# Performance work log

Measured on AMD Instinct MI355X. Metric: run time of the kernel, lower is better.

Reference implementation:

```python
import jax, jax.numpy as jnp
import numpy as np

B, N, E = 2, 2048, 1024   # batch, seq_len, embed_dim (= hidden_dim)
H, HD = 16, 64            # num_heads, head_dim


def setup_inputs() -> dict:
    key = jax.random.key(0)
    ks = jax.random.split(key, 6)
    w = lambda k: jax.random.normal(k, (E, E), jnp.float32) * 0.02
    return {
        "x": jax.random.normal(ks[0], (B, N, E), jnp.float32),
        "Wq": w(ks[1]), "bq": jnp.zeros((E,), jnp.float32),
        "Wk": w(ks[2]), "bk": jnp.zeros((E,), jnp.float32),
        "Wv": w(ks[3]), "bv": jnp.zeros((E,), jnp.float32),
        "Wu": w(ks[4]), "bu": jnp.zeros((E,), jnp.float32),
        "Wo": w(ks[5]), "bo": jnp.zeros((E,), jnp.float32),
        "ln_g": jnp.ones((E,), jnp.float32),
        "ln_b": jnp.zeros((E,), jnp.float32),
    }


def reference(x, Wq, bq, Wk, bk, Wv, bv, Wu, bu, Wo, bo, ln_g, ln_b):
    # projections (torch Linear: x @ W.T + b)
    q = x @ Wq.T + bq
    k = x @ Wk.T + bk
    v = jax.nn.silu(x @ Wv.T + bv)   # uv_act = swish
    u = jax.nn.silu(x @ Wu.T + bu)
    # split heads: [B, N, H*HD] -> [B, H, N, HD]
    split = lambda t: t.reshape(B, N, H, HD).transpose(0, 2, 1, 3)
    q, k, v = split(q), split(k), split(v)
    # non-softmax attention: ReLU on scaled energy (no causal mask)
    energy = jnp.einsum("bhnd,bhmd->bhnm", q, k) / jnp.float32(np.sqrt(HD))
    energy = jax.nn.relu(energy)
    out = jnp.einsum("bhnm,bhmd->bhnd", energy, v)
    # merge heads: [B, H, N, HD] -> [B, N, H*HD]
    out = out.transpose(0, 2, 1, 3).reshape(B, N, H * HD)
    # layernorm over hidden_dim
    mu = out.mean(-1, keepdims=True)
    var = out.var(-1, keepdims=True)
    out = (out - mu) * jax.lax.rsqrt(var + 1e-5) * ln_g + ln_b
    # gate and output projection
    out = u * out
    return out @ Wo.T + bo
```

## Files before the change

kernel.cpp:

```cpp
#include <hip/hip_runtime.h>
#include <stdint.h>

typedef unsigned short u16;
typedef __attribute__((ext_vector_type(8))) short short8;
typedef __attribute__((ext_vector_type(4))) short short4v;
typedef __attribute__((ext_vector_type(4))) float floatx4;
typedef __attribute__((ext_vector_type(4))) int intx4;

#define B_ 2
#define N_ 2048
#define E_ 1024
#define H_ 16
#define HD_ 64
#define M_TOT (B_ * N_)

__device__ __forceinline__ float bf2f(u16 h) {
    union { unsigned u; float f; } c; c.u = ((unsigned)h) << 16; return c.f;
}
__device__ __forceinline__ u16 f2bf(float f) {
    union { float f; unsigned u; } c; c.f = f;
    unsigned r = c.u + 0x7FFFu + ((c.u >> 16) & 1u);
    return (u16)(r >> 16);
}
__device__ __forceinline__ float silu_f(float x) { return x / (1.f + __expf(-x)); }

template <typename T> __device__ __forceinline__ void store_out(T* p, float v);
template <> __device__ __forceinline__ void store_out<u16>(u16* p, float v)    { *p = f2bf(v); }
template <> __device__ __forceinline__ void store_out<float>(float* p, float v) { *p = v; }

__device__ __forceinline__ void gll16(const void* g, void* l) {
    __builtin_amdgcn_global_load_lds(
        (const __attribute__((address_space(1))) void*)g,
        (__attribute__((address_space(3))) void*)l,
        16, 0, 0);
}

#if __has_builtin(__builtin_amdgcn_mfma_f32_16x16x16bf16_1k)
__device__ __forceinline__ floatx4 mfma16(short4v a, short4v b, floatx4 c) {
    return __builtin_amdgcn_mfma_f32_16x16x16bf16_1k(a, b, c, 0, 0, 0);
}
#else
__device__ __forceinline__ floatx4 mfma16(short4v a, short4v b, floatx4 c) {
    floatx4 d;
    asm volatile("v_mfma_f32_16x16x16_bf16 %0, %1, %2, %3\n\ts_nop 3"
                 : "=v"(d) : "v"(a), "v"(b), "v"(c));
    return d;
}
#endif

__device__ __forceinline__ short4v relu_pack(floatx4 s) {
    union { float f; unsigned u; } c0, c1, c2, c3;
    c0.f = fmaxf(s[0], 0.f); c1.f = fmaxf(s[1], 0.f);
    c2.f = fmaxf(s[2], 0.f); c3.f = fmaxf(s[3], 0.f);
    unsigned lo = __builtin_amdgcn_perm(c1.u + 0x8000u, c0.u + 0x8000u, 0x07060302);
    unsigned hi = __builtin_amdgcn_perm(c3.u + 0x8000u, c2.u + 0x8000u, 0x07060302);
    union { unsigned v[2]; short4v s4; } r; r.v[0] = lo; r.v[1] = hi;
    return r.s4;
}

__launch_bounds__(256, 4)
__global__ void cvt6(const float* __restrict__ s0, const float* __restrict__ s1,
                     const float* __restrict__ s2, const float* __restrict__ s3,
                     const float* __restrict__ s4, const float* __restrict__ s5,
                     u16* __restrict__ d0, u16* __restrict__ d1,
                     u16* __restrict__ d2, u16* __restrict__ d3,
                     u16* __restrict__ d4, u16* __restrict__ d5)
{
    const int z = blockIdx.z;
    if (z > 0 && blockIdx.x >= E_ * E_ / 2048) return;
    const float* src = (z == 0) ? s0 : (z == 1) ? s1 : (z == 2) ? s2
                     : (z == 3) ? s3 : (z == 4) ? s4 : s5;
    u16* dst         = (z == 0) ? d0 : (z == 1) ? d1 : (z == 2) ? d2
                     : (z == 3) ? d3 : (z == 4) ? d4 : d5;
    const int i = (blockIdx.x * 256 + threadIdx.x) * 8;
    floatx4 a = *(const floatx4*)(src + i);
    floatx4 b = *(const floatx4*)(src + i + 4);
    union { u16 h[8]; intx4 v; } o;
    o.h[0] = f2bf(a[0]); o.h[1] = f2bf(a[1]); o.h[2] = f2bf(a[2]); o.h[3] = f2bf(a[3]);
    o.h[4] = f2bf(b[0]); o.h[5] = f2bf(b[1]); o.h[6] = f2bf(b[2]); o.h[7] = f2bf(b[3]);
    *(intx4*)(dst + i) = o.v;
}

template <typename OutT>
__launch_bounds__(256, 2)
__global__ void gemm4(const u16* __restrict__ A,
                      const u16* __restrict__ W0, const u16* __restrict__ W1,
                      const u16* __restrict__ W2, const u16* __restrict__ W3,
                      const float* __restrict__ bi0, const float* __restrict__ bi1,
                      const float* __restrict__ bi2, const float* __restrict__ bi3,
                      OutT* __restrict__ O0, OutT* __restrict__ O1,
                      OutT* __restrict__ O2, OutT* __restrict__ O3,
                      int actmask, int scalemask, int K)
{
    __shared__ u16 a_lds[128 * 32];
    __shared__ u16 b_lds[128 * 32];

    const int z = blockIdx.z;
    const u16* W    = (z == 0) ? W0 : (z == 1) ? W1 : (z == 2) ? W2 : W3;
    const float* Bi = (z == 0) ? bi0 : (z == 1) ? bi1 : (z == 2) ? bi2 : bi3;
    OutT* Out       = (z == 0) ? O0 : (z == 1) ? O1 : (z == 2) ? O2 : O3;
    const bool act = (actmask >> z) & 1;
    const float osc = ((scalemask >> z) & 1) ? 0.125f : 1.0f;

    const int t    = threadIdx.x;
    const int wave = t >> 6, lane = t & 63, quad = lane >> 4, l16 = lane & 15;
    const int wm = wave >> 1, wn = wave & 1;
    const int m0 = blockIdx.y * 128;
    const int n0 = blockIdx.x * 128;

    floatx4 acc[4][4];
    const floatx4 fz = {0.f, 0.f, 0.f, 0.f};
    for (int i = 0; i < 4; i++)
        for (int j = 0; j < 4; j++) acc[i][j] = fz;

    const int ar = t >> 2;
    const int ac = (t & 3) * 8;
    const u16* Ag0 = A + (size_t)(m0 + ar) * K + ac;
    const u16* Ag1 = A + (size_t)(m0 + 64 + ar) * K + ac;
    const u16* Bg0 = W + (size_t)(n0 + ar) * K + ac;
    const u16* Bg1 = W + (size_t)(n0 + 64 + ar) * K + ac;
    u16* al0 = a_lds + wave * 512;
    u16* al1 = a_lds + 2048 + wave * 512;
    u16* bl0 = b_lds + wave * 512;
    u16* bl1 = b_lds + 2048 + wave * 512;

    for (int k0 = 0; k0 < K; k0 += 32) {
        __syncthreads();
        gll16(Ag0 + k0, al0);
        gll16(Ag1 + k0, al1);
        gll16(Bg0 + k0, bl0);
        gll16(Bg1 + k0, bl1);
        __syncthreads();

        short8 af[4], bfr[4];
        for (int i = 0; i < 4; i++)
            af[i]  = *(const short8*)&a_lds[(wm * 64 + i * 16 + l16) * 32 + quad * 8];
        for (int j = 0; j < 4; j++)
            bfr[j] = *(const short8*)&b_lds[(wn * 64 + j * 16 + l16) * 32 + quad * 8];
        for (int i = 0; i < 4; i++)
            for (int j = 0; j < 4; j++)
                acc[i][j] = __builtin_amdgcn_mfma_f32_16x16x32_bf16(af[i], bfr[j], acc[i][j], 0, 0, 0);
    }

    float bias_v[4];
    for (int j = 0; j < 4; j++) bias_v[j] = Bi[n0 + wn * 64 + j * 16 + l16];

    for (int i = 0; i < 4; i++) {
        const int row = m0 + wm * 64 + i * 16 + quad * 4;
        for (int j = 0; j < 4; j++) {
            const int col = n0 + wn * 64 + j * 16 + l16;
            for (int r = 0; r < 4; r++) {
                float v = acc[i][j][r] + bias_v[j];
                if (act) v = silu_f(v);
                v *= osc;
                store_out<OutT>(&Out[(size_t)(row + r) * E_ + col], v);
            }
        }
    }
}

__launch_bounds__(256, 4)
__global__ void vtrans(const u16* __restrict__ V, u16* __restrict__ VT)
{
    __shared__ u16 ts[64 * 72];
    const int bh = blockIdx.y;
    const int b = bh >> 4, h = bh & 15;
    const int n0 = blockIdx.x * 64;
    const int t = threadIdx.x;
    const int r = t >> 2, seg = (t & 3) * 16;

    const u16* src = V + ((size_t)b * N_ + n0 + r) * E_ + h * HD_ + seg;
    intx4 x0 = *(const intx4*)(src);
    intx4 x1 = *(const intx4*)(src + 8);
    *(intx4*)&ts[r * 72 + seg]     = x0;
    *(intx4*)&ts[r * 72 + seg + 8] = x1;
    __syncthreads();

    union { u16 h[16]; intx4 v[2]; } buf;
    for (int j = 0; j < 16; j++) buf.h[j] = ts[(seg + j) * 72 + r];
    u16* dst = VT + ((size_t)bh * HD_ + r) * N_ + n0 + seg;
    *(intx4*)(dst)     = buf.v[0];
    *(intx4*)(dst + 8) = buf.v[1];
}

#define LQ 72
#define KSPLIT 2
#define KCHUNK (N_ / KSPLIT)

__launch_bounds__(256, 4)
__global__ void attn(const u16* __restrict__ Q, const u16* __restrict__ Kk,
                     const u16* __restrict__ VT,
                     float* __restrict__ Oa0, float* __restrict__ Oa1)
{
    __shared__ u16 k_lds[64 * LQ];
    __shared__ u16 vt_lds[64 * LQ];

    const int bh = blockIdx.y;
    const int b = bh >> 4, h = bh & 15;
    const int z = blockIdx.z;
    float* __restrict__ Oa = (z == 0) ? Oa0 : Oa1;
    const int key_base = z * KCHUNK;

    const int t = threadIdx.x;
    const int wave = t >> 6, lane = t & 63, quad = lane >> 4, l16 = lane & 15;
    const int q0 = blockIdx.x * 128 + wave * 32;
    const size_t base = (size_t)b * N_ * E_ + h * HD_;

    short8 aq[2][2];
    for (int mi = 0; mi < 2; mi++)
        for (int ks = 0; ks < 2; ks++)
            aq[mi][ks] = *(const short8*)(Q + base + (size_t)(q0 + mi * 16 + l16) * E_ + ks * 32 + quad * 8);

    floatx4 o[2][4];
    const floatx4 fz = {0.f, 0.f, 0.f, 0.f};
    for (int mi = 0; mi < 2; mi++)
        for (int n = 0; n < 4; n++) o[mi][n] = fz;

    const int srow = t >> 2;
    const int sseg = (t & 3) * 16;
    const u16* Ksrc = Kk + base + (size_t)(key_base + srow) * E_ + sseg;
    const u16* Vsrc = VT + ((size_t)bh * HD_ + srow) * N_ + key_base + sseg;

    for (int kt = 0; kt < KCHUNK / 64; kt++) {
        __syncthreads();
        intx4 k0v = *(const intx4*)(Ksrc + (size_t)(kt * 64) * E_);
        intx4 k1v = *(const intx4*)(Ksrc + (size_t)(kt * 64) * E_ + 8);
        intx4 v0v = *(const intx4*)(Vsrc + kt * 64);
        intx4 v1v = *(const intx4*)(Vsrc + kt * 64 + 8);
        *(intx4*)&k_lds[srow * LQ + sseg]      = k0v;
        *(intx4*)&k_lds[srow * LQ + sseg + 8]  = k1v;
        *(intx4*)&vt_lds[srow * LQ + sseg]     = v0v;
        *(intx4*)&vt_lds[srow * LQ + sseg + 8] = v1v;
        __syncthreads();

        for (int n = 0; n < 4; n++) {
            short8 ka0 = *(const short8*)&k_lds[(n * 16 + l16) * LQ + quad * 8];
            short8 ka1 = *(const short8*)&k_lds[(n * 16 + l16) * LQ + 32 + quad * 8];
            short4v bv[4];
            for (int nd = 0; nd < 4; nd++)
                bv[nd] = *(const short4v*)&vt_lds[(nd * 16 + l16) * LQ + n * 16 + quad * 4];

            for (int mi = 0; mi < 2; mi++) {
                floatx4 st = __builtin_amdgcn_mfma_f32_16x16x32_bf16(ka0, aq[mi][0], fz, 0, 0, 0);
                st = __builtin_amdgcn_mfma_f32_16x16x32_bf16(ka1, aq[mi][1], st, 0, 0, 0);
                short4v sa = relu_pack(st);
                for (int nd = 0; nd < 4; nd++)
                    o[mi][nd] = mfma16(sa, bv[nd], o[mi][nd]);
            }
        }
    }

    for (int mi = 0; mi < 2; mi++)
        for (int n = 0; n < 4; n++)
            for (int r = 0; r < 4; r++)
                Oa[(size_t)(b * N_ + q0 + mi * 16 + quad * 4 + r) * E_ + h * HD_ + n * 16 + l16] = o[mi][n][r];
}

__launch_bounds__(256, 4)
__global__ void ln_gate(const float* __restrict__ A0, const float* __restrict__ A1,
                        const u16* __restrict__ U,
                        const float* __restrict__ G, const float* __restrict__ Bb,
                        u16* __restrict__ Out)
{
    const int row = blockIdx.x;
    const int t = threadIdx.x;
    const floatx4 v0 = *(const floatx4*)(A0 + (size_t)row * E_ + t * 4);
    const floatx4 v1 = *(const floatx4*)(A1 + (size_t)row * E_ + t * 4);
    floatx4 v;
    for (int i = 0; i < 4; i++) v[i] = v0[i] + v1[i];
    float s  = v[0] + v[1] + v[2] + v[3];
    float ss = v[0] * v[0] + v[1] * v[1] + v[2] * v[2] + v[3] * v[3];
    for (int off = 32; off; off >>= 1) {
        s  += __shfl_down(s, off, 64);
        ss += __shfl_down(ss, off, 64);
    }
    __shared__ float red[8];
    const int wave = t >> 6, lane = t & 63;
    if (lane == 0) { red[wave] = s; red[4 + wave] = ss; }
    __syncthreads();
    const float S  = red[0] + red[1] + red[2] + red[3];
    const float SS = red[4] + red[5] + red[6] + red[7];
    const float mu  = S * (1.f / E_);
    const float var = SS * (1.f / E_) - mu * mu;
    const float rstd = rsqrtf(var + 1e-5f);

    short4v outv;
    for (int i = 0; i < 4; i++) {
        const int e = t * 4 + i;
        float y = (v[i] - mu) * rstd * G[e] + Bb[e];
        y *= bf2f(U[(size_t)row * E_ + e]);
        outv[i] = (short)f2bf(y);
    }
    *(short4v*)(Out + (size_t)row * E_ + t * 4) = outv;
}

extern "C" void kernel_launch(void* const* d_in, const int* in_sizes, int n_in,
                              void* d_out, int out_size, void* d_ws, size_t ws_size,
                              hipStream_t stream)
{
    const float* x   = (const float*)d_in[0];
    const float* Wq  = (const float*)d_in[1];
    const float* bq  = (const float*)d_in[2];
    const float* Wk  = (const float*)d_in[3];
    const float* bk  = (const float*)d_in[4];
    const float* Wv  = (const float*)d_in[5];
    const float* bv  = (const float*)d_in[6];
    const float* Wu  = (const float*)d_in[7];
    const float* bu  = (const float*)d_in[8];
    const float* Wo  = (const float*)d_in[9];
    const float* bo  = (const float*)d_in[10];
    const float* lng = (const float*)d_in[11];
    const float* lnb = (const float*)d_in[12];

    char* ws = (char*)d_ws;
    u16*  qw  = (u16*)(ws);
    u16*  kw  = (u16*)(ws + 8388608);
    u16*  vw  = (u16*)(ws + 16777216);
    u16*  uw  = (u16*)(ws + 25165824);
    float* aw = (float*)(ws + 33554432);
    u16*  xb  = (u16*)(ws + 50331648);
    u16*  vt  = (u16*)(ws + 50331648);
    u16*  wbq = (u16*)(ws + 58720256);
    u16*  wbk = (u16*)(ws + 60817408);
    u16*  wbv = (u16*)(ws + 62914560);
    u16*  wbu = (u16*)(ws + 65011712);
    u16*  wbo = (u16*)(ws + 67108864);
    u16*  gw  = (u16*)(ws);

    float* out = (float*)d_out;

    const dim3 blk(256, 1, 1);

    cvt6<<<dim3(M_TOT * E_ / 2048, 1, 6), blk, 0, stream>>>(
        x, Wq, Wk, Wv, Wu, Wo, xb, wbq, wbk, wbv, wbu, wbo);
    gemm4<u16><<<dim3(8, 32, 4), blk, 0, stream>>>(xb, wbq, wbk, wbv, wbu,
                                                   bq, bk, bv, bu,
                                                   qw, kw, vw, uw, 0xC, 0x1, E_);
    vtrans<<<dim3(N_ / 64, B_ * H_, 1), blk, 0, stream>>>(vw, vt);
    attn<<<dim3(N_ / 128, B_ * H_, KSPLIT), blk, 0, stream>>>(qw, kw, vt, aw, out);
    ln_gate<<<dim3(M_TOT, 1, 1), blk, 0, stream>>>(aw, out, uw, lng, lnb, gw);
    gemm4<float><<<dim3(8, 32, 1), blk, 0, stream>>>(gw, wbo, wbo, wbo, wbo,
                                                     bo, bo, bo, bo,
                                                     out, out, out, out, 0x0, 0x0, E_);
}
```

Measured before the change: 235.9 us.

## Store K and V in MFMA-fragment tiled layouts from projection GEMM, drop vtrans

The projection GEMM epilogue now writes K and V directly into per-(head, key-tile) blocks laid out in MFMA fragment order. This removes the separate V transpose kernel and lets attention load tiles with contiguous global-to-LDS copies and conflict-free fragment reads. Attention also doubles the query rows per block (64 per wave), so each K/V tile is reused more, at the cost of more registers and lower occupancy (launch bound 2). The GEMM epilogue for K/V now does scattered 2-byte stores, which may hurt write coalescing.

```diff
diff --git a/kernel.cpp b/kernel.cpp
--- a/kernel.cpp
+++ b/kernel.cpp
@@ -90,7 +90,7 @@
                       const float* __restrict__ bi2, const float* __restrict__ bi3,
                       OutT* __restrict__ O0, OutT* __restrict__ O1,
                       OutT* __restrict__ O2, OutT* __restrict__ O3,
-                      int actmask, int scalemask, int K)
+                      int actmask, int scalemask, int kt2z, int vt2z, int K)
 {
     __shared__ u16 a_lds[128 * 32];
     __shared__ u16 b_lds[128 * 32];
@@ -101,6 +101,7 @@
     OutT* Out       = (z == 0) ? O0 : (z == 1) ? O1 : (z == 2) ? O2 : O3;
     const bool act = (actmask >> z) & 1;
     const float osc = ((scalemask >> z) & 1) ? 0.125f : 1.0f;
+    const int mode = (z == kt2z) ? 1 : (z == vt2z) ? 2 : 0;
 
     const int t    = threadIdx.x;
     const int wave = t >> 6, lane = t & 63, quad = lane >> 4, l16 = lane & 15;
@@ -146,101 +147,94 @@
     for (int j = 0; j < 4; j++) bias_v[j] = Bi[n0 + wn * 64 + j * 16 + l16];
 
     for (int i = 0; i < 4; i++) {
-        const int row = m0 + wm * 64 + i * 16 + quad * 4;
         for (int j = 0; j < 4; j++) {
             const int col = n0 + wn * 64 + j * 16 + l16;
             for (int r = 0; r < 4; r++) {
+                const int row = m0 + wm * 64 + i * 16 + quad * 4 + r;
                 float v = acc[i][j][r] + bias_v[j];
                 if (act) v = silu_f(v);
                 v *= osc;
-                store_out<OutT>(&Out[(size_t)(row + r) * E_ + col], v);
+                size_t idx;
+                if (mode == 1) {
+                    const int b = row >> 11, seq = row & 2047;
+                    const int h = col >> 6, d = col & 63;
+                    const int bh = b * 16 + h;
+                    const int kt = seq >> 6, n = (seq >> 4) & 3, l16k = seq & 15;
+                    const int ks = d >> 5, qd = (d >> 3) & 3, jj = d & 7;
+                    idx = ((size_t)(bh * 32 + kt) * 8 + n * 2 + ks) * 512
+                        + (qd * 16 + l16k) * 8 + jj;
+                } else if (mode == 2) {
+                    const int b = row >> 11, seq = row & 2047;
+                    const int h = col >> 6, d = col & 63;
+                    const int bh = b * 16 + h;
+                    const int kt = seq >> 6, n = (seq >> 4) & 3;
+                    const int qv = (seq >> 2) & 3, jv = seq & 3;
+                    const int nd = d >> 4, l16v = d & 15;
+                    idx = ((size_t)(bh * 32 + kt) * 16 + n * 4 + nd) * 256
+                        + (qv * 16 + l16v) * 4 + jv;
+                } else {
+                    idx = (size_t)row * E_ + col;
+                }
+                store_out<OutT>(&Out[idx], v);
             }
         }
     }
 }
 
-__launch_bounds__(256, 4)
-__global__ void vtrans(const u16* __restrict__ V, u16* __restrict__ VT)
-{
-    __shared__ u16 ts[64 * 72];
-    const int bh = blockIdx.y;
-    const int b = bh >> 4, h = bh & 15;
-    const int n0 = blockIdx.x * 64;
-    const int t = threadIdx.x;
-    const int r = t >> 2, seg = (t & 3) * 16;
-
-    const u16* src = V + ((size_t)b * N_ + n0 + r) * E_ + h * HD_ + seg;
-    intx4 x0 = *(const intx4*)(src);
-    intx4 x1 = *(const intx4*)(src + 8);
-    *(intx4*)&ts[r * 72 + seg]     = x0;
-    *(intx4*)&ts[r * 72 + seg + 8] = x1;
-    __syncthreads();
-
-    union { u16 h[16]; intx4 v[2]; } buf;
-    for (int j = 0; j < 16; j++) buf.h[j] = ts[(seg + j) * 72 + r];
-    u16* dst = VT + ((size_t)bh * HD_ + r) * N_ + n0 + seg;
-    *(intx4*)(dst)     = buf.v[0];
-    *(intx4*)(dst + 8) = buf.v[1];
-}
-
-#define LQ 72
 #define KSPLIT 2
 #define KCHUNK (N_ / KSPLIT)
 
-__launch_bounds__(256, 4)
-__global__ void attn(const u16* __restrict__ Q, const u16* __restrict__ Kk,
-                     const u16* __restrict__ VT,
+__launch_bounds__(256, 2)
+__global__ void attn(const u16* __restrict__ Q, const u16* __restrict__ KT2,
+                     const u16* __restrict__ VT2,
                      float* __restrict__ Oa0, float* __restrict__ Oa1)
 {
-    __shared__ u16 k_lds[64 * LQ];
-    __shared__ u16 vt_lds[64 * LQ];
+    __shared__ u16 k_lds[4096];
+    __shared__ u16 v_lds[4096];
 
     const int bh = blockIdx.y;
     const int b = bh >> 4, h = bh & 15;
     const int z = blockIdx.z;
     float* __restrict__ Oa = (z == 0) ? Oa0 : Oa1;
-    const int key_base = z * KCHUNK;
 
     const int t = threadIdx.x;
     const int wave = t >> 6, lane = t & 63, quad = lane >> 4, l16 = lane & 15;
-    const int q0 = blockIdx.x * 128 + wave * 32;
+    const int q0 = blockIdx.x * 256 + wave * 64;
     const size_t base = (size_t)b * N_ * E_ + h * HD_;
 
-    short8 aq[2][2];
-    for (int mi = 0; mi < 2; mi++)
+    short8 aq[4][2];
+    for (int mi = 0; mi < 4; mi++)
         for (int ks = 0; ks < 2; ks++)
             aq[mi][ks] = *(const short8*)(Q + base + (size_t)(q0 + mi * 16 + l16) * E_ + ks * 32 + quad * 8);
 
-    floatx4 o[2][4];
+    floatx4 o[4][4];
     const floatx4 fz = {0.f, 0.f, 0.f, 0.f};
-    for (int mi = 0; mi < 2; mi++)
-        for (int n = 0; n < 4; n++) o[mi][n] = fz;
-
-    const int srow = t >> 2;
-    const int sseg = (t & 3) * 16;
-    const u16* Ksrc = Kk + base + (size_t)(key_base + srow) * E_ + sseg;
-    const u16* Vsrc = VT + ((size_t)bh * HD_ + srow) * N_ + key_base + sseg;
+    for (int mi = 0; mi < 4; mi++)
+        for (int nd = 0; nd < 4; nd++) o[mi][nd] = fz;
+
+    const u16* Ksrc = KT2 + ((size_t)bh * 32 + z * (KCHUNK / 64)) * 4096 + t * 8;
+    const u16* Vsrc = VT2 + ((size_t)bh * 32 + z * (KCHUNK / 64)) * 4096 + t * 8;
+    u16* kl = k_lds + wave * 512;
+    u16* vl = v_lds + wave * 512;
 
     for (int kt = 0; kt < KCHUNK / 64; kt++) {
         __syncthreads();
-        intx4 k0v = *(const intx4*)(Ksrc + (size_t)(kt * 64) * E_);
-        intx4 k1v = *(const intx4*)(Ksrc + (size_t)(kt * 64) * E_ + 8);
-        intx4 v0v = *(const intx4*)(Vsrc + kt * 64);
-        intx4 v1v = *(const intx4*)(Vsrc + kt * 64 + 8);
-        *(intx4*)&k_lds[srow * LQ + sseg]      = k0v;
-        *(intx4*)&k_lds[srow * LQ + sseg + 8]  = k1v;
-        *(intx4*)&vt_lds[srow * LQ + sseg]     = v0v;
-        *(intx4*)&vt_lds[srow * LQ + sseg + 8] = v1v;
+        const u16* kg = Ksrc + (size_t)kt * 4096;
+        const u16* vg = Vsrc + (size_t)kt * 4096;
+        gll16(kg, kl);
+        gll16(kg + 2048, kl + 2048);
+        gll16(vg, vl);
+        gll16(vg + 2048, vl + 2048);
         __syncthreads();
 
         for (int n = 0; n < 4; n++) {
-            short8 ka0 = *(const short8*)&k_lds[(n * 16 + l16) * LQ + quad * 8];
-            short8 ka1 = *(const short8*)&k_lds[(n * 16 + l16) * LQ + 32 + quad * 8];
+            short8 ka0 = *(const short8*)&k_lds[(n * 2 + 0) * 512 + lane * 8];
+            short8 ka1 = *(const short8*)&k_lds[(n * 2 + 1) * 512 + lane * 8];
             short4v bv[4];
             for (int nd = 0; nd < 4; nd++)
-                bv[nd] = *(const short4v*)&vt_lds[(nd * 16 + l16) * LQ + n * 16 + quad * 4];
-
-            for (int mi = 0; mi < 2; mi++) {
+                bv[nd] = *(const short4v*)&v_lds[(n * 4 + nd) * 256 + lane * 4];
+
+            for (int mi = 0; mi < 4; mi++) {
                 floatx4 st = __builtin_amdgcn_mfma_f32_16x16x32_bf16(ka0, aq[mi][0], fz, 0, 0, 0);
                 st = __builtin_amdgcn_mfma_f32_16x16x32_bf16(ka1, aq[mi][1], st, 0, 0, 0);
                 short4v sa = relu_pack(st);
@@ -250,10 +244,10 @@
         }
     }
 
-    for (int mi = 0; mi < 2; mi++)
-        for (int n = 0; n < 4; n++)
+    for (int mi = 0; mi < 4; mi++)
+        for (int nd = 0; nd < 4; nd++)
             for (int r = 0; r < 4; r++)
-                Oa[(size_t)(b * N_ + q0 + mi * 16 + quad * 4 + r) * E_ + h * HD_ + n * 16 + l16] = o[mi][n][r];
+                Oa[(size_t)(b * N_ + q0 + mi * 16 + quad * 4 + r) * E_ + h * HD_ + nd * 16 + l16] = o[mi][nd][r];
 }
 
 __launch_bounds__(256, 4)
@@ -319,7 +313,6 @@
     u16*  uw  = (u16*)(ws + 25165824);
     float* aw = (float*)(ws + 33554432);
     u16*  xb  = (u16*)(ws + 50331648);
-    u16*  vt  = (u16*)(ws + 50331648);
     u16*  wbq = (u16*)(ws + 58720256);
     u16*  wbk = (u16*)(ws + 60817408);
     u16*  wbv = (u16*)(ws + 62914560);
@@ -335,11 +328,12 @@
         x, Wq, Wk, Wv, Wu, Wo, xb, wbq, wbk, wbv, wbu, wbo);
     gemm4<u16><<<dim3(8, 32, 4), blk, 0, stream>>>(xb, wbq, wbk, wbv, wbu,
                                                    bq, bk, bv, bu,
-                                                   qw, kw, vw, uw, 0xC, 0x1, E_);
-    vtrans<<<dim3(N_ / 64, B_ * H_, 1), blk, 0, stream>>>(vw, vt);
-    attn<<<dim3(N_ / 128, B_ * H_, KSPLIT), blk, 0, stream>>>(qw, kw, vt, aw, out);
+                                                   qw, kw, vw, uw,
+                                                   0xC, 0x1, 1, 2, E_);
+    attn<<<dim3(N_ / 256, B_ * H_, KSPLIT), blk, 0, stream>>>(qw, kw, vw, aw, out);
     ln_gate<<<dim3(M_TOT, 1, 1), blk, 0, stream>>>(aw, out, uw, lng, lnb, gw);
     gemm4<float><<<dim3(8, 32, 1), blk, 0, stream>>>(gw, wbo, wbo, wbo, wbo,
                                                      bo, bo, bo, bo,
-                                                     out, out, out, out, 0x0, 0x0, E_);
-}
+                                                     out, out, out, out,
+                                                     0x0, 0x0, -1, -1, E_);
+}
```

Result: slower. 611.7 us (+159.3%).
